# Kernel optimization log

Hardware: AMD Instinct MI355X
Metric: run time of the kernel (lower is better)

The kernel has to match this reference:

```python
import jax, jax.numpy as jnp
import numpy as np

NUM_ITERS = 20  # fixed in the original forward: transcribe(dna, iterations=20)


def transcribe(dna_seed, dna_a, dna_b):
    """Fractal DNA decompression: 20 elementwise contractive-map iterations
    over the full weight tensor, starting from the DNA seed."""
    def step(w, ab):
        a, b = ab
        w = a * w + b * jnp.sin(w)
        return w, None
    w, _ = jax.lax.scan(step, dna_seed, (dna_a, dna_b))
    return w  # [out_features, in_features]


def setup_inputs() -> dict:
    key = jax.random.key(0)
    k1, k2, k3, k4, k5 = jax.random.split(key, 5)
    TOKENS, IN_F, OUT_F = 2048, 4096, 4096
    return {
        "x": jax.random.normal(k1, (TOKENS, IN_F), dtype=jnp.float32),
        "dna_seed": jax.random.normal(k2, (OUT_F, IN_F), dtype=jnp.float32),
        "dna_a": jax.random.uniform(k3, (NUM_ITERS,), dtype=jnp.float32),
        "dna_b": jax.random.uniform(k4, (NUM_ITERS,), dtype=jnp.float32),
        "bias": jax.random.normal(k5, (OUT_F,), dtype=jnp.float32),
    }


def reference(x, dna_seed, dna_a, dna_b, bias):
    weight = transcribe(dna_seed, dna_a, dna_b)          # [out, in]
    # F.linear(x, weight, bias) == x @ weight.T + bias
    return jnp.einsum('ti,oi->to', x, weight) + bias     # [tokens, out]
```

## Files before the change

kernel.cpp:

```cpp
#include <hip/hip_runtime.h>

typedef __attribute__((ext_vector_type(8))) short short8;
typedef __attribute__((ext_vector_type(4))) float floatx4;

#define TOKENS 2048
#define IN_F   4096
#define OUT_F  4096
#define NITER  20
#define BK     64

#define INV_2PI 0.15915494309189535f
#define TWO_PI  6.283185307179586f

__device__ __forceinline__ unsigned short f2bf(float f) {
    unsigned int u = __builtin_bit_cast(unsigned int, f);
    u += 0x7fffu + ((u >> 16) & 1u);
    return (unsigned short)(u >> 16);
}

__device__ __forceinline__ void step4(float4& v, float a, float bc) {
    v.x = __builtin_fmaf(bc, __builtin_amdgcn_sinf(v.x), a * v.x);
    v.y = __builtin_fmaf(bc, __builtin_amdgcn_sinf(v.y), a * v.y);
    v.z = __builtin_fmaf(bc, __builtin_amdgcn_sinf(v.z), a * v.z);
    v.w = __builtin_fmaf(bc, __builtin_amdgcn_sinf(v.w), a * v.w);
}

#define WBLOCKS (OUT_F * IN_F / 8 / 256)
#define XBLOCKS (TOKENS * IN_F / 8 / 256)

__global__ __launch_bounds__(256) void transcribe_fused_kernel(
    const float4* __restrict__ seed, const float4* __restrict__ xin,
    const float* __restrict__ da, const float* __restrict__ db,
    short8* __restrict__ w_out, short8* __restrict__ x_out)
{
    const int b = blockIdx.x;
    short8 o;
    if (b < WBLOCKS) {
        int i = b * 256 + threadIdx.x;
        float4 u = seed[2 * i];
        float4 v = seed[2 * i + 1];
        u.x *= INV_2PI; u.y *= INV_2PI; u.z *= INV_2PI; u.w *= INV_2PI;
        v.x *= INV_2PI; v.y *= INV_2PI; v.z *= INV_2PI; v.w *= INV_2PI;
#pragma unroll
        for (int t = 0; t < NITER; t++) {
            float a = da[t], bc = db[t] * INV_2PI;
            step4(u, a, bc);
            step4(v, a, bc);
        }
        o[0] = (short)f2bf(u.x * TWO_PI); o[1] = (short)f2bf(u.y * TWO_PI);
        o[2] = (short)f2bf(u.z * TWO_PI); o[3] = (short)f2bf(u.w * TWO_PI);
        o[4] = (short)f2bf(v.x * TWO_PI); o[5] = (short)f2bf(v.y * TWO_PI);
        o[6] = (short)f2bf(v.z * TWO_PI); o[7] = (short)f2bf(v.w * TWO_PI);
        w_out[i] = o;
    } else {
        int i = (b - WBLOCKS) * 256 + threadIdx.x;
        float4 u = xin[2 * i];
        float4 v = xin[2 * i + 1];
        o[0] = (short)f2bf(u.x); o[1] = (short)f2bf(u.y);
        o[2] = (short)f2bf(u.z); o[3] = (short)f2bf(u.w);
        o[4] = (short)f2bf(v.x); o[5] = (short)f2bf(v.y);
        o[6] = (short)f2bf(v.z); o[7] = (short)f2bf(v.w);
        x_out[i] = o;
    }
}

__device__ __forceinline__ void g2l16(const ushort* g, ushort* l) {
    __builtin_amdgcn_global_load_lds(
        (const __attribute__((address_space(1))) unsigned int*)g,
        (__attribute__((address_space(3))) unsigned int*)l, 16, 0, 0);
}

__global__ __launch_bounds__(256, 2) void gemm_bt_kernel(
    const ushort* __restrict__ A,
    const ushort* __restrict__ B,
    const float* __restrict__ bias,
    float* __restrict__ C)
{
    __shared__ ushort As[2][128 * BK];
    __shared__ ushort Bs[2][128 * BK];

    const int tid  = threadIdx.x;
    const int lane = tid & 63;
    const int wid  = tid >> 6;
    const int bn   = blockIdx.x;
    const int bm   = blockIdx.y;
    const int wm   = (wid >> 1) << 6;
    const int wn   = (wid & 1) << 6;
    const int fm   = lane & 15;
    const int q    = lane >> 4;

    const int gcol = (((lane & 7) ^ (lane >> 3)) << 3);

    const ushort* gA = A + (size_t)(bm * 128) * IN_F;
    const ushort* gB = B + (size_t)(bn * 128) * IN_F;

    floatx4 acc[4][4];
#pragma unroll
    for (int i = 0; i < 4; i++)
#pragma unroll
        for (int j = 0; j < 4; j++)
            acc[i][j] = (floatx4){0.f, 0.f, 0.f, 0.f};

#define STAGE(k0v, bufi)                                                      \
    {                                                                         \
        _Pragma("unroll")                                                     \
        for (int u = 0; u < 4; u++) {                                         \
            const int cb = ((u << 2) | wid) << 6;             \
            const int r  = (cb >> 3) + (lane >> 3);           \
            g2l16(gA + (size_t)r * IN_F + (k0v) + gcol,                       \
                  &As[bufi][cb * 8 + lane * 8]);                              \
            g2l16(gB + (size_t)r * IN_F + (k0v) + gcol,                       \
                  &Bs[bufi][cb * 8 + lane * 8]);                              \
        }                                                                     \
    }

#define COMPUTE(bufi)                                                         \
    {                                                                         \
        _Pragma("unroll")                                                     \
        for (int s = 0; s < 2; s++) {                                         \
            short8 af[4], bf[4];                                              \
            const int sa = (((q + 4 * s) & 7) ^ (fm & 7)) << 3;               \
            _Pragma("unroll")                                                 \
            for (int i = 0; i < 4; i++) {                                     \
                af[i] = *(const short8*)&As[bufi][(wm + i * 16 + fm) * BK + sa]; \
                bf[i] = *(const short8*)&Bs[bufi][(wn + i * 16 + fm) * BK + sa]; \
            }                                                                 \
            _Pragma("unroll")                                                 \
            for (int i = 0; i < 4; i++)                                       \
                _Pragma("unroll")                                             \
                for (int j = 0; j < 4; j++)                                   \
                    acc[i][j] = __builtin_amdgcn_mfma_f32_16x16x32_bf16(      \
                        af[i], bf[j], acc[i][j], 0, 0, 0);                    \
        }                                                                     \
    }

    STAGE(0, 0);
    __syncthreads();
    STAGE(BK, 1);
    COMPUTE(0);
    __syncthreads();
    for (int k0 = 2 * BK; k0 < IN_F; k0 += 2 * BK) {
        STAGE(k0, 0);
        COMPUTE(1);
        __syncthreads();
        STAGE(k0 + BK, 1);
        COMPUTE(0);
        __syncthreads();
    }
    COMPUTE(1);

#undef STAGE
#undef COMPUTE

    const int cn = lane & 15;
    const int cm = (lane >> 4) << 2;
    float bv[4];
#pragma unroll
    for (int j = 0; j < 4; j++)
        bv[j] = bias[bn * 128 + wn + j * 16 + cn];
#pragma unroll
    for (int i = 0; i < 4; i++) {
#pragma unroll
        for (int r = 0; r < 4; r++) {
            int m = bm * 128 + wm + i * 16 + cm + r;
            float* crow = C + (size_t)m * OUT_F + bn * 128 + wn + cn;
#pragma unroll
            for (int j = 0; j < 4; j++)
                crow[j * 16] = acc[i][j][r] + bv[j];
        }
    }
}

extern "C" void kernel_launch(void* const* d_in, const int* in_sizes, int n_in,
                              void* d_out, int out_size, void* d_ws, size_t ws_size,
                              hipStream_t stream) {
    const float* x    = (const float*)d_in[0];
    const float* seed = (const float*)d_in[1];
    const float* da   = (const float*)d_in[2];
    const float* db   = (const float*)d_in[3];
    const float* bias = (const float*)d_in[4];
    float* out        = (float*)d_out;

    ushort* w_bf = (ushort*)d_ws;
    ushort* x_bf = w_bf + (size_t)OUT_F * IN_F;

    transcribe_fused_kernel<<<WBLOCKS + XBLOCKS, 256, 0, stream>>>(
        (const float4*)seed, (const float4*)x, da, db,
        (short8*)w_bf, (short8*)x_bf);

    dim3 grid(OUT_F / 128, TOKENS / 128);
    gemm_bt_kernel<<<grid, 256, 0, stream>>>(x_bf, w_bf, bias, out);
}
```

Baseline: 214.8 us.

## Use 256x128 GEMM tiles with 512 threads and triple-buffered LDS pipeline

Restructures the bf16 GEMM to use 256x128 block tiles with 8 waves, a three-stage LDS ring buffer fed by direct global-to-LDS loads, and explicit vmcnt waits with a single barrier per half-tile. It also adds a block-index swizzle so neighbouring blocks share operand rows, and raises MFMA issue priority with s_setprio. The aim is better overlap of global loads with MFMA work and more data reuse per block. In exchange it needs 144 KB of dynamic LDS, set through a function attribute, and relies on hand-placed waitcnt counts being correct.

```diff
diff --git a/kernel.cpp b/kernel.cpp
--- a/kernel.cpp
+++ b/kernel.cpp
@@ -7,7 +7,6 @@
 #define IN_F   4096
 #define OUT_F  4096
 #define NITER  20
-#define BK     64
 
 #define INV_2PI 0.15915494309189535f
 #define TWO_PI  6.283185307179586f
@@ -70,29 +69,42 @@
         (__attribute__((address_space(3))) unsigned int*)l, 16, 0, 0);
 }
 
-__global__ __launch_bounds__(256, 2) void gemm_bt_kernel(
+#define BK     64
+#define BM     256
+#define BN     128
+#define NT     (IN_F / BK)
+#define ASLOT  (BM * BK)
+#define BSLOT  (BN * BK)
+#define LDS_BYTES (3 * (ASLOT + BSLOT) * 2)
+
+__global__ __launch_bounds__(512, 2) void gemm_bt_kernel(
     const ushort* __restrict__ A,
     const ushort* __restrict__ B,
     const float* __restrict__ bias,
     float* __restrict__ C)
 {
-    __shared__ ushort As[2][128 * BK];
-    __shared__ ushort Bs[2][128 * BK];
+    extern __shared__ ushort lds[];
+    ushort* As = lds;
+    ushort* Bs = lds + 3 * ASLOT;
 
     const int tid  = threadIdx.x;
     const int lane = tid & 63;
     const int wid  = tid >> 6;
-    const int bn   = blockIdx.x;
-    const int bm   = blockIdx.y;
-    const int wm   = (wid >> 1) << 6;
-    const int wn   = (wid & 1) << 6;
-    const int fm   = lane & 15;
-    const int q    = lane >> 4;
+
+    const int bid = blockIdx.x;
+    const int swz = (bid & 7) * 32 + (bid >> 3);
+    const int bn  = swz & 31;
+    const int bm  = swz >> 5;
+
+    const int wm = (wid >> 1) << 6;
+    const int wn = (wid & 1) << 6;
+    const int fm = lane & 15;
+    const int q  = lane >> 4;
 
     const int gcol = (((lane & 7) ^ (lane >> 3)) << 3);
 
-    const ushort* gA = A + (size_t)(bm * 128) * IN_F;
-    const ushort* gB = B + (size_t)(bn * 128) * IN_F;
+    const ushort* gA = A + (size_t)(bm * BM) * IN_F;
+    const ushort* gB = B + (size_t)(bn * BN) * IN_F;
 
     floatx4 acc[4][4];
 #pragma unroll
@@ -101,69 +113,112 @@
         for (int j = 0; j < 4; j++)
             acc[i][j] = (floatx4){0.f, 0.f, 0.f, 0.f};
 
-#define STAGE(k0v, bufi)                                                      \
+#define STAGE(k0v, sl)                                                        \
     {                                                                         \
         _Pragma("unroll")                                                     \
         for (int u = 0; u < 4; u++) {                                         \
-            const int cb = ((u << 2) | wid) << 6;             \
-            const int r  = (cb >> 3) + (lane >> 3);           \
+            const int cb = ((u << 3) | wid) << 6;                             \
+            const int r  = (cb >> 3) + (lane >> 3);                           \
             g2l16(gA + (size_t)r * IN_F + (k0v) + gcol,                       \
-                  &As[bufi][cb * 8 + lane * 8]);                              \
+                  As + (sl) * ASLOT + cb * 8 + lane * 8);                     \
+        }                                                                     \
+        _Pragma("unroll")                                                     \
+        for (int u = 0; u < 2; u++) {                                         \
+            const int cb = ((u << 3) | wid) << 6;                             \
+            const int r  = (cb >> 3) + (lane >> 3);                           \
             g2l16(gB + (size_t)r * IN_F + (k0v) + gcol,                       \
-                  &Bs[bufi][cb * 8 + lane * 8]);                              \
-        }                                                                     \
-    }
-
-#define COMPUTE(bufi)                                                         \
+                  Bs + (sl) * BSLOT + cb * 8 + lane * 8);                     \
+        }                                                                     \
+    }
+
+#define LOADFRAG(s_, sl)                                                      \
+    const int sa = (((q + 4 * (s_)) & 7) ^ (fm & 7)) << 3;                    \
+    _Pragma("unroll")                                                         \
+    for (int i = 0; i < 4; i++) {                                             \
+        af[i] = *(const short8*)(As + (sl) * ASLOT + (wm + i * 16 + fm) * BK + sa); \
+        bf[i] = *(const short8*)(Bs + (sl) * BSLOT + (wn + i * 16 + fm) * BK + sa); \
+    }
+
+#define MFMA16()                                                              \
+    __builtin_amdgcn_s_setprio(1);                                            \
+    _Pragma("unroll")                                                         \
+    for (int i = 0; i < 4; i++)                                               \
+        _Pragma("unroll")                                                     \
+        for (int j = 0; j < 4; j++)                                           \
+            acc[i][j] = __builtin_amdgcn_mfma_f32_16x16x32_bf16(              \
+                af[i], bf[j], acc[i][j], 0, 0, 0);                            \
+    __builtin_amdgcn_s_setprio(0);
+
+#define TILE_MAIN(vm, sl, k3)                                                 \
     {                                                                         \
-        _Pragma("unroll")                                                     \
-        for (int s = 0; s < 2; s++) {                                         \
-            short8 af[4], bf[4];                                              \
-            const int sa = (((q + 4 * s) & 7) ^ (fm & 7)) << 3;               \
-            _Pragma("unroll")                                                 \
-            for (int i = 0; i < 4; i++) {                                     \
-                af[i] = *(const short8*)&As[bufi][(wm + i * 16 + fm) * BK + sa]; \
-                bf[i] = *(const short8*)&Bs[bufi][(wn + i * 16 + fm) * BK + sa]; \
-            }                                                                 \
-            _Pragma("unroll")                                                 \
-            for (int i = 0; i < 4; i++)                                       \
-                _Pragma("unroll")                                             \
-                for (int j = 0; j < 4; j++)                                   \
-                    acc[i][j] = __builtin_amdgcn_mfma_f32_16x16x32_bf16(      \
-                        af[i], bf[j], acc[i][j], 0, 0, 0);                    \
-        }                                                                     \
-    }
-
-    STAGE(0, 0);
-    __syncthreads();
-    STAGE(BK, 1);
-    COMPUTE(0);
-    __syncthreads();
-    for (int k0 = 2 * BK; k0 < IN_F; k0 += 2 * BK) {
-        STAGE(k0, 0);
-        COMPUTE(1);
-        __syncthreads();
-        STAGE(k0 + BK, 1);
-        COMPUTE(0);
-        __syncthreads();
-    }
-    COMPUTE(1);
+        asm volatile("s_waitcnt vmcnt(" #vm ")" ::: "memory");                \
+        __builtin_amdgcn_s_barrier();                                         \
+        {                                                                     \
+            short8 af[4], bf[4];                                              \
+            LOADFRAG(0, sl);                                                  \
+            MFMA16();                                                         \
+        }                                                                     \
+        {                                                                     \
+            short8 af[4], bf[4];                                              \
+            LOADFRAG(1, sl);                                                  \
+            asm volatile("s_waitcnt lgkmcnt(0)" ::: "memory");                \
+            __builtin_amdgcn_s_barrier();                                     \
+            STAGE(k3, sl);                                                    \
+            __builtin_amdgcn_sched_barrier(0);                                \
+            MFMA16();                                                         \
+        }                                                                     \
+    }
+
+#define TILE_TAIL(vm, sl)                                                     \
+    {                                                                         \
+        asm volatile("s_waitcnt vmcnt(" #vm ")" ::: "memory");                \
+        __builtin_amdgcn_s_barrier();                                         \
+        {                                                                     \
+            short8 af[4], bf[4];                                              \
+            LOADFRAG(0, sl);                                                  \
+            MFMA16();                                                         \
+        }                                                                     \
+        {                                                                     \
+            short8 af[4], bf[4];                                              \
+            LOADFRAG(1, sl);                                                  \
+            MFMA16();                                                         \
+        }                                                                     \
+    }
+
+    STAGE(0 * BK, 0);
+    STAGE(1 * BK, 1);
+    STAGE(2 * BK, 2);
+
+    int st   = 0;
+    int kpre = 3 * BK;
+#pragma unroll 1
+    for (int t = 0; t <= NT - 4; ++t) {
+        TILE_MAIN(12, st, kpre);
+        kpre += BK;
+        st = (st == 2) ? 0 : st + 1;
+    }
+    TILE_TAIL(12, 1);
+    TILE_TAIL(6, 2);
+    TILE_TAIL(0, 0);
 
 #undef STAGE
-#undef COMPUTE
+#undef LOADFRAG
+#undef MFMA16
+#undef TILE_MAIN
+#undef TILE_TAIL
 
     const int cn = lane & 15;
     const int cm = (lane >> 4) << 2;
     float bv[4];
 #pragma unroll
     for (int j = 0; j < 4; j++)
-        bv[j] = bias[bn * 128 + wn + j * 16 + cn];
+        bv[j] = bias[bn * BN + wn + j * 16 + cn];
 #pragma unroll
     for (int i = 0; i < 4; i++) {
 #pragma unroll
         for (int r = 0; r < 4; r++) {
-            int m = bm * 128 + wm + i * 16 + cm + r;
-            float* crow = C + (size_t)m * OUT_F + bn * 128 + wn + cn;
+            int m = bm * BM + wm + i * 16 + cm + r;
+            float* crow = C + (size_t)m * OUT_F + bn * BN + wn + cn;
 #pragma unroll
             for (int j = 0; j < 4; j++)
                 crow[j * 16] = acc[i][j][r] + bv[j];
@@ -184,10 +239,18 @@
     ushort* w_bf = (ushort*)d_ws;
     ushort* x_bf = w_bf + (size_t)OUT_F * IN_F;
 
+    static bool lds_attr_set = false;
+    if (!lds_attr_set) {
+        hipFuncSetAttribute(reinterpret_cast<const void*>(gemm_bt_kernel),
+                            hipFuncAttributeMaxDynamicSharedMemorySize,
+                            LDS_BYTES);
+        lds_attr_set = true;
+    }
+
     transcribe_fused_kernel<<<WBLOCKS + XBLOCKS, 256, 0, stream>>>(
         (const float4*)seed, (const float4*)x, da, db,
         (short8*)w_bf, (short8*)x_bf);
 
-    dim3 grid(OUT_F / 128, TOKENS / 128);
-    gemm_bt_kernel<<<grid, 256, 0, stream>>>(x_bf, w_bf, bias, out);
-}
+    gemm_bt_kernel<<<dim3(32 * 8), dim3(512), LDS_BYTES, stream>>>(
+        x_bf, w_bf, bias, out);
+}
```

New measurement: 207.4 us. -3.4%, faster.
